# Kernel tuning notes

Measured on AMD Instinct MI355X. Metric: run time of the kernel, lower is better.

The kernel has to match this reference:

```python
import jax, jax.numpy as jnp
import numpy as np

DIM = 256
NPOINT = 64      # fps sample count (hardcoded in forward)
NSAMPLE = 8      # ball-query neighbors
RADIUS = 4.0
LN_EPS = 1e-5


def _fps(coor, K):
    # coor: [B,N,3] -> idx [B,K] int32, pointnet2-style (start at index 0)
    B, N, _ = coor.shape
    def step(carry, _):
        dists, far = carry
        c = jnp.take_along_axis(coor, far[:, None, None], axis=1)  # [B,1,3]
        d = jnp.sum((coor - c) ** 2, axis=-1)                      # [B,N]
        dists = jnp.minimum(dists, d)
        nxt = jnp.argmax(dists, axis=-1).astype(jnp.int32)
        return (dists, nxt), far
    init = (jnp.full((B, N), 1e10, coor.dtype), jnp.zeros((B,), jnp.int32))
    _, idx = jax.lax.scan(step, init, None, length=K)
    return idx.T  # [B,K]


def _ball_query(coor, centers, radius, nsample):
    # coor [B,N,3], centers [B,S,3] -> idx [B,S,nsample] (first-nsample within radius,
    # padded with the first hit, CUDA ball_query semantics)
    d2 = jnp.sum((centers[:, :, None, :] - coor[:, None, :, :]) ** 2, axis=-1)  # [B,S,N]
    mask = d2 < radius * radius
    cum = jnp.cumsum(mask.astype(jnp.int32), axis=-1)
    idxs, founds = [], []
    for j in range(nsample):  # fixed tiny loop
        sel = (cum == j + 1) & mask
        idxs.append(jnp.argmax(sel, axis=-1))
        founds.append(jnp.any(sel, axis=-1))
    idx = jnp.stack(idxs, axis=-1)       # [B,S,ns]
    found = jnp.stack(founds, axis=-1)
    return jnp.where(found, idx, idx[..., :1])


def _layernorm(v, g, b):
    m = jnp.mean(v, axis=-1, keepdims=True)
    var = jnp.mean((v - m) ** 2, axis=-1, keepdims=True)
    return (v - m) * jax.lax.rsqrt(var + LN_EPS) * g + b


def setup_inputs() -> dict:
    key = jax.random.key(0)
    ks = jax.random.split(key, 4)
    B, N = 8, 32768
    x = jax.random.normal(ks[0], (B, N, DIM), jnp.float32)
    coor = jax.random.normal(ks[1], (B, N, 3), jnp.float32)
    s = 1.0 / np.sqrt(DIM)
    Wq = jax.random.normal(ks[2], (DIM, DIM), jnp.float32) * s
    Wk = jax.random.normal(ks[3], (DIM, DIM), jnp.float32) * s
    return {
        "x": x, "coor": coor, "Wq": Wq, "Wk": Wk,
        "ln_q_g": jnp.ones((DIM,), jnp.float32), "ln_q_b": jnp.zeros((DIM,), jnp.float32),
        "ln_k_g": jnp.ones((DIM,), jnp.float32), "ln_k_b": jnp.zeros((DIM,), jnp.float32),
    }


def reference(x, coor, Wq, Wk, ln_q_g, ln_q_b, ln_k_g, ln_k_b):
    B, N, C = x.shape
    S = NPOINT
    bidx = jnp.arange(B)[:, None, None]

    fps_idx = _fps(coor, S)                              # [B,S]
    sample_coor = jnp.take_along_axis(coor, fps_idx[..., None], axis=1)  # [B,S,3]
    sample_x = jnp.take_along_axis(x, fps_idx[..., None], axis=1)        # [B,S,C]

    nidx = _ball_query(coor, sample_coor, RADIUS, NSAMPLE)  # [B,S,ns]
    grouped_xyz = coor[bidx, nidx]                          # [B,S,ns,3]
    grouped_feat = x[bidx, nidx]                            # [B,S,ns,C]
    local_coor = grouped_xyz - sample_coor[:, :, None, :]   # relative xyz [B,S,ns,3]

    global_x = jnp.max(grouped_feat, axis=2)                # [B,S,C]
    diff_x = global_x - sample_x                            # [B,S,C]
    diff_coor = jnp.mean(local_coor, axis=2)                # [B,S,3]

    # faithful reproduction of torch's view(B, NK, heads, -1) on a [B,3,S] tensor
    v = jnp.transpose(diff_coor, (0, 2, 1)).reshape(B, S, 3)  # memory reinterpretation

    q = _layernorm(diff_x, ln_q_g, ln_q_b) @ Wq.T           # [B,S,C]
    k = _layernorm(sample_x, ln_k_g, ln_k_b) @ Wk.T         # [B,S,C]
    scale = 1.0 / np.sqrt(DIM)  # head_dim = out_dim // 1
    attn = jax.nn.softmax(jnp.einsum('bnc,bmc->bnm', q, k) * scale, axis=-1)
    coor_2 = jnp.einsum('bnm,bmd->bnd', attn, v)            # [B,S,3]

    return (sample_x + diff_x, sample_coor + coor_2)
```

## Files before the change

### kernel.cpp

```cpp
#include <hip/hip_runtime.h>

#define BATCH 8
#define NPTS  32768
#define DIM   256
#define NSAMP 64
#define NNBR  8
#define LN_EPS 1e-5f

#define K_LDS    12
#define K_REG    12
#define K_STREAM 8

__device__ float g_sample_coor[BATCH * NSAMP * 3];
__device__ float g_diff_coor[BATCH * NSAMP * 3];
__device__ float g_qbuf[BATCH * NSAMP * DIM];
__device__ float g_kbuf[BATCH * NSAMP * DIM];
__device__ int   g_fidx[BATCH * NSAMP];


__device__ __forceinline__ double dist2_64(float px, float py, float pz,
                                           float cx, float cy, float cz) {
    double dx = (double)px - (double)cx;
    double dy = (double)py - (double)cy;
    double dz = (double)pz - (double)cz;
    return (dx * dx + dy * dy) + dz * dz;
}

__global__ __launch_bounds__(1024, 4) void fps_kernel(
    const float* __restrict__ coor)
{
    const int b = blockIdx.x;
    const int t = threadIdx.x;
    const float* cb = coor + (size_t)b * NPTS * 3;

    __shared__ float s_coor[K_LDS][1024][3];
    __shared__ float s_rv[16];
    __shared__ int   s_ri[16];
    __shared__ float s_ctr[3];

#pragma unroll
    for (int k = 0; k < K_LDS; ++k) {
        const int p = (k << 10) + t;
        s_coor[k][t][0] = cb[p * 3 + 0];
        s_coor[k][t][1] = cb[p * 3 + 1];
        s_coor[k][t][2] = cb[p * 3 + 2];
    }
    float px[K_REG], py[K_REG], pz[K_REG];
#pragma unroll
    for (int k = 0; k < K_REG; ++k) {
        const int p = ((K_LDS + k) << 10) + t;
        px[k] = cb[p * 3 + 0];
        py[k] = cb[p * 3 + 1];
        pz[k] = cb[p * 3 + 2];
    }

    float dist[32];
#pragma unroll
    for (int k = 0; k < 32; ++k) dist[k] = 1e10f;

    float cx = cb[0], cy = cb[1], cz = cb[2];
    int cidx = 0;
    __syncthreads();

    for (int s = 0; s < NSAMP; ++s) {
        if (t == 0) {
            g_fidx[b * NSAMP + s] = cidx;
            g_sample_coor[(b * NSAMP + s) * 3 + 0] = cx;
            g_sample_coor[(b * NSAMP + s) * 3 + 1] = cy;
            g_sample_coor[(b * NSAMP + s) * 3 + 2] = cz;
        }
        if (s == NSAMP - 1) break;

        float best = -1.0f; int bidx = 0;

#pragma unroll
        for (int k = 0; k < K_LDS; ++k) {
            float dx = s_coor[k][t][0] - cx;
            float dy = s_coor[k][t][1] - cy;
            float dz = s_coor[k][t][2] - cz;
            float d2 = dx * dx + dy * dy + dz * dz;
            float nd = fminf(dist[k], d2);
            dist[k] = nd;
            if (nd > best) { best = nd; bidx = (k << 10) + t; }
        }
#pragma unroll
        for (int k = 0; k < K_REG; ++k) {
            float dx = px[k] - cx;
            float dy = py[k] - cy;
            float dz = pz[k] - cz;
            float d2 = dx * dx + dy * dy + dz * dz;
            float nd = fminf(dist[K_LDS + k], d2);
            dist[K_LDS + k] = nd;
            if (nd > best) { best = nd; bidx = ((K_LDS + k) << 10) + t; }
        }
#pragma unroll 2
        for (int k = 0; k < K_STREAM; ++k) {
            const int p = ((K_LDS + K_REG + k) << 10) + t;
            float sx = cb[p * 3 + 0];
            float sy = cb[p * 3 + 1];
            float sz = cb[p * 3 + 2];
            float dx = sx - cx, dy = sy - cy, dz = sz - cz;
            float d2 = dx * dx + dy * dy + dz * dz;
            float nd = fminf(dist[K_LDS + K_REG + k], d2);
            dist[K_LDS + K_REG + k] = nd;
            if (nd > best) { best = nd; bidx = p; }
        }

#pragma unroll
        for (int off = 32; off > 0; off >>= 1) {
            float ov = __shfl_xor(best, off);
            int   oi = __shfl_xor(bidx, off);
            if (ov > best || (ov == best && oi < bidx)) { best = ov; bidx = oi; }
        }
        if ((t & 63) == 0) { s_rv[t >> 6] = best; s_ri[t >> 6] = bidx; }
        __syncthreads();

        if (t < 64) {
            float bv = (t < 16) ? s_rv[t] : -2.0f;
            int   bi = (t < 16) ? s_ri[t] : 0x7fffffff;
#pragma unroll
            for (int off = 8; off > 0; off >>= 1) {
                float ov = __shfl_xor(bv, off);
                int   oi = __shfl_xor(bi, off);
                if (ov > bv || (ov == bv && oi < bi)) { bv = ov; bi = oi; }
            }
            if (t == 0) {
                cidx = bi;
                s_ctr[0] = cb[bi * 3 + 0];
                s_ctr[1] = cb[bi * 3 + 1];
                s_ctr[2] = cb[bi * 3 + 2];
            }
        }
        __syncthreads();
        cx = s_ctr[0]; cy = s_ctr[1]; cz = s_ctr[2];
    }
}

__global__ __launch_bounds__(64) void ballquery_kernel(
    const float* __restrict__ coor,
    const float* __restrict__ x,
    float* __restrict__ out0)
{
    const int bid = blockIdx.x;
    const int b = bid >> 6, s = bid & 63;
    const int lane = threadIdx.x;
    const float* cb = coor + (size_t)b * NPTS * 3;

    const float cx = g_sample_coor[(b * NSAMP + s) * 3 + 0];
    const float cy = g_sample_coor[(b * NSAMP + s) * 3 + 1];
    const float cz = g_sample_coor[(b * NSAMP + s) * 3 + 2];

    __shared__ int s_nidx[NNBR];
    int found = 0;
    for (int ch = 0; ch < NPTS / 64 && found < NNBR; ++ch) {
        int p = (ch << 6) + lane;
        double d2 = dist2_64(cb[p * 3 + 0], cb[p * 3 + 1], cb[p * 3 + 2],
                             cx, cy, cz);
        unsigned long long m = __ballot(d2 < 16.0);
        while (m && found < NNBR) {
            int bpos = __ffsll(m) - 1;
            if (lane == 0) s_nidx[found] = (ch << 6) + bpos;
            ++found;
            m &= m - 1;
        }
    }
    if (lane == 0) {
        if (found == 0) { s_nidx[0] = 0; found = 1; }
        int f0 = s_nidx[0];
        for (int j = found; j < NNBR; ++j) s_nidx[j] = f0;
    }
    __syncthreads();

    int c0 = lane * 4;
    float a0 = -1e30f, a1 = -1e30f, a2 = -1e30f, a3 = -1e30f;
#pragma unroll
    for (int j = 0; j < NNBR; ++j) {
        const float4 v = *(const float4*)(x + ((size_t)b * NPTS + s_nidx[j]) * DIM + c0);
        a0 = fmaxf(a0, v.x); a1 = fmaxf(a1, v.y);
        a2 = fmaxf(a2, v.z); a3 = fmaxf(a3, v.w);
    }
    float4 o; o.x = a0; o.y = a1; o.z = a2; o.w = a3;
    *(float4*)(out0 + ((size_t)(b * NSAMP + s)) * DIM + c0) = o;

    if (lane < 3) {
        float sum = 0.f;
#pragma unroll
        for (int j = 0; j < NNBR; ++j) {
            float pv = cb[s_nidx[j] * 3 + lane];
            sum += pv - ((lane == 0) ? cx : (lane == 1) ? cy : cz);
        }
        g_diff_coor[(b * NSAMP + s) * 3 + lane] = sum * 0.125f;
    }
}

__global__ __launch_bounds__(256) void ln_gemm_kernel(
    const float* __restrict__ x,
    const float* __restrict__ out0,
    const float* __restrict__ Wq,
    const float* __restrict__ Wk,
    const float* __restrict__ gq, const float* __restrict__ bq,
    const float* __restrict__ gk, const float* __restrict__ bk)
{
    const int bid = blockIdx.x;
    const int which = bid & 1;
    const int s = (bid >> 1) & 63;
    const int b = bid >> 7;
    const int c = threadIdx.x;

    const int fidx = g_fidx[b * NSAMP + s];
    float xs = x[((size_t)b * NPTS + fidx) * DIM + c];
    float r  = which ? xs : (out0[(size_t)(b * NSAMP + s) * DIM + c] - xs);

    __shared__ float red[4];
    __shared__ float ln[DIM];

    float sum = r;
#pragma unroll
    for (int off = 32; off; off >>= 1) sum += __shfl_xor(sum, off);
    int wid = c >> 6;
    if ((c & 63) == 0) red[wid] = sum;
    __syncthreads();
    float mean = (red[0] + red[1] + red[2] + red[3]) * (1.0f / DIM);
    float d = r - mean;
    float vs = d * d;
#pragma unroll
    for (int off = 32; off; off >>= 1) vs += __shfl_xor(vs, off);
    __syncthreads();
    if ((c & 63) == 0) red[wid] = vs;
    __syncthreads();
    float var = (red[0] + red[1] + red[2] + red[3]) * (1.0f / DIM);
    float rs = 1.0f / sqrtf(var + LN_EPS);

    ln[c] = d * rs * (which ? gk[c] : gq[c]) + (which ? bk[c] : bq[c]);
    __syncthreads();

    const float* W = (which ? Wk : Wq) + (size_t)c * DIM;
    float acc = 0.f;
#pragma unroll 4
    for (int i = 0; i < DIM; i += 4) {
        float4 wv = *(const float4*)(W + i);
        acc = fmaf(ln[i + 0], wv.x, acc);
        acc = fmaf(ln[i + 1], wv.y, acc);
        acc = fmaf(ln[i + 2], wv.z, acc);
        acc = fmaf(ln[i + 3], wv.w, acc);
    }
    (which ? g_kbuf : g_qbuf)[(size_t)(b * NSAMP + s) * DIM + c] = acc;
}

__global__ __launch_bounds__(1024) void attn_kernel(
    float* __restrict__ out1)
{
    const int b = blockIdx.x;
    const int tid = threadIdx.x;
    __shared__ float att[64][64];
    __shared__ float vv[64][3];

    {
        const int i  = tid >> 4;
        const int j0 = (tid & 15) << 2;
        const float* qr = g_qbuf + (size_t)(b * NSAMP + i) * DIM;
        const float* k0 = g_kbuf + (size_t)(b * NSAMP + j0) * DIM;
        float a0 = 0, a1 = 0, a2 = 0, a3 = 0;
        for (int ii = 0; ii < DIM; ii += 4) {
            float4 qv = *(const float4*)(qr + ii);
            float4 v0 = *(const float4*)(k0 + ii);
            float4 v1 = *(const float4*)(k0 + DIM + ii);
            float4 v2 = *(const float4*)(k0 + 2 * DIM + ii);
            float4 v3 = *(const float4*)(k0 + 3 * DIM + ii);
            a0 += qv.x * v0.x + qv.y * v0.y + qv.z * v0.z + qv.w * v0.w;
            a1 += qv.x * v1.x + qv.y * v1.y + qv.z * v1.z + qv.w * v1.w;
            a2 += qv.x * v2.x + qv.y * v2.y + qv.z * v2.z + qv.w * v2.w;
            a3 += qv.x * v3.x + qv.y * v3.y + qv.z * v3.z + qv.w * v3.w;
        }
        att[i][j0 + 0] = a0 * 0.0625f;
        att[i][j0 + 1] = a1 * 0.0625f;
        att[i][j0 + 2] = a2 * 0.0625f;
        att[i][j0 + 3] = a3 * 0.0625f;
    }
    __syncthreads();

    const int wv_ = tid >> 6, lane = tid & 63;
    for (int r = wv_; r < 64; r += 16) {
        float v = att[r][lane];
        float m = v;
#pragma unroll
        for (int off = 32; off; off >>= 1) m = fmaxf(m, __shfl_xor(m, off));
        float e = expf(v - m);
        float ss = e;
#pragma unroll
        for (int off = 32; off; off >>= 1) ss += __shfl_xor(ss, off);
        att[r][lane] = e / ss;
    }
    if (tid < 192) {
        int m = tid / 3, d = tid - 3 * m;
        vv[m][d] = g_diff_coor[(size_t)(b * NSAMP + (tid & 63)) * 3 + (tid >> 6)];
    }
    __syncthreads();

    for (int r = wv_; r < 64; r += 16) {
        float a = att[r][lane];
        float s0 = a * vv[lane][0];
        float s1 = a * vv[lane][1];
        float s2 = a * vv[lane][2];
#pragma unroll
        for (int off = 32; off; off >>= 1) {
            s0 += __shfl_xor(s0, off);
            s1 += __shfl_xor(s1, off);
            s2 += __shfl_xor(s2, off);
        }
        if (lane == 0) {
            int o = (b * NSAMP + r) * 3;
            out1[o + 0] = g_sample_coor[o + 0] + s0;
            out1[o + 1] = g_sample_coor[o + 1] + s1;
            out1[o + 2] = g_sample_coor[o + 2] + s2;
        }
    }
}

extern "C" void kernel_launch(void* const* d_in, const int* in_sizes, int n_in,
                              void* d_out, int out_size, void* d_ws, size_t ws_size,
                              hipStream_t stream)
{
    const float* x    = (const float*)d_in[0];
    const float* coor = (const float*)d_in[1];
    if (in_sizes[0] == BATCH * NPTS * 3) {
        x    = (const float*)d_in[1];
        coor = (const float*)d_in[0];
    }
    const float* Wq   = (const float*)d_in[2];
    const float* Wk   = (const float*)d_in[3];
    const float* gq   = (const float*)d_in[4];
    const float* bq   = (const float*)d_in[5];
    const float* gk   = (const float*)d_in[6];
    const float* bk   = (const float*)d_in[7];

    float* out0 = (float*)d_out;
    float* out1 = out0 + (size_t)BATCH * NSAMP * DIM;

    hipLaunchKernelGGL(fps_kernel, dim3(BATCH), dim3(1024), 0, stream, coor);
    hipLaunchKernelGGL(ballquery_kernel, dim3(BATCH * NSAMP), dim3(64), 0, stream,
                       coor, x, out0);
    hipLaunchKernelGGL(ln_gemm_kernel, dim3(BATCH * NSAMP * 2), dim3(256), 0, stream,
                       x, out0, Wq, Wk, gq, bq, gk, bk);
    hipLaunchKernelGGL(attn_kernel, dim3(BATCH), dim3(1024), 0, stream, out1);
}
```

Before: 748.6 us.

## Stream FPS tail points with float4 loads instead of register caching

The farthest point sampling kernel no longer keeps 12 points per thread cached in registers. It now streams 20 points per thread from global memory on every iteration, using three float4 loads that cover four contiguous points per thread. A waves-per-EU attribute is added to pin occupancy. This frees registers and vectorises the loads, but each sampling iteration now reads more global or L2 data on a latency-bound serial loop.

Measured after the change: 1.116 ms. 49.0% more time.

```diff
diff --git a/kernel.cpp b/kernel.cpp
--- a/kernel.cpp
+++ b/kernel.cpp
@@ -8,8 +8,7 @@
 #define LN_EPS 1e-5f
 
 #define K_LDS    12
-#define K_REG    12
-#define K_STREAM 8
+#define K_STREAM 20
 
 __device__ float g_sample_coor[BATCH * NSAMP * 3];
 __device__ float g_diff_coor[BATCH * NSAMP * 3];
@@ -26,8 +25,9 @@
     return (dx * dx + dy * dy) + dz * dz;
 }
 
-__global__ __launch_bounds__(1024, 4) void fps_kernel(
-    const float* __restrict__ coor)
+__global__ __launch_bounds__(1024, 4)
+__attribute__((amdgpu_waves_per_eu(4, 4)))
+void fps_kernel(const float* __restrict__ coor)
 {
     const int b = blockIdx.x;
     const int t = threadIdx.x;
@@ -45,18 +45,12 @@
         s_coor[k][t][1] = cb[p * 3 + 1];
         s_coor[k][t][2] = cb[p * 3 + 2];
     }
-    float px[K_REG], py[K_REG], pz[K_REG];
-#pragma unroll
-    for (int k = 0; k < K_REG; ++k) {
-        const int p = ((K_LDS + k) << 10) + t;
-        px[k] = cb[p * 3 + 0];
-        py[k] = cb[p * 3 + 1];
-        pz[k] = cb[p * 3 + 2];
-    }
 
     float dist[32];
 #pragma unroll
     for (int k = 0; k < 32; ++k) dist[k] = 1e10f;
+
+    const float4* cb4 = (const float4*)(cb + 3 * (K_LDS << 10));
 
     float cx = cb[0], cy = cb[1], cz = cb[2];
     int cidx = 0;
@@ -83,27 +77,25 @@
             dist[k] = nd;
             if (nd > best) { best = nd; bidx = (k << 10) + t; }
         }
-#pragma unroll
-        for (int k = 0; k < K_REG; ++k) {
-            float dx = px[k] - cx;
-            float dy = py[k] - cy;
-            float dz = pz[k] - cz;
-            float d2 = dx * dx + dy * dy + dz * dz;
-            float nd = fminf(dist[K_LDS + k], d2);
-            dist[K_LDS + k] = nd;
-            if (nd > best) { best = nd; bidx = ((K_LDS + k) << 10) + t; }
-        }
 #pragma unroll 2
-        for (int k = 0; k < K_STREAM; ++k) {
-            const int p = ((K_LDS + K_REG + k) << 10) + t;
-            float sx = cb[p * 3 + 0];
-            float sy = cb[p * 3 + 1];
-            float sz = cb[p * 3 + 2];
-            float dx = sx - cx, dy = sy - cy, dz = sz - cz;
-            float d2 = dx * dx + dy * dy + dz * dz;
-            float nd = fminf(dist[K_LDS + K_REG + k], d2);
-            dist[K_LDS + K_REG + k] = nd;
-            if (nd > best) { best = nd; bidx = p; }
+        for (int j = 0; j < 5; ++j) {
+            const int g = (j << 10) + t;
+            const float4 v0 = cb4[g * 3 + 0];
+            const float4 v1 = cb4[g * 3 + 1];
+            const float4 v2 = cb4[g * 3 + 2];
+            const float qx[4] = { v0.x, v0.w, v1.z, v2.y };
+            const float qy[4] = { v0.y, v1.x, v1.w, v2.z };
+            const float qz[4] = { v0.z, v1.y, v2.x, v2.w };
+            const int pbase = (K_LDS << 10) + (g << 2);
+#pragma unroll
+            for (int i = 0; i < 4; ++i) {
+                float dx = qx[i] - cx, dy = qy[i] - cy, dz = qz[i] - cz;
+                float d2 = dx * dx + dy * dy + dz * dz;
+                const int di = K_LDS + (j << 2) + i;
+                float nd = fminf(dist[di], d2);
+                dist[di] = nd;
+                if (nd > best) { best = nd; bidx = pbase + i; }
+            }
         }
 
 #pragma unroll
```

## Split ball query into parallel mask pass and gather, streamline FPS reduction

Applied to the files above, without the earlier changes.

Ball query is split into two kernels. The first computes per-sample radius bitmasks across all point chunks in parallel (4096 blocks). The second scans those masks to find the first neighbours and gathers the features. This removes the serial per-sample chunk scan with its dependent global loads. FPS drops the register-cached points, moves one more slice into LDS and streams the rest from global. It also replaces the second barrier with a redundant all-thread final reduction that uses double-buffered shared slots, and reads the chosen centre from LDS. The cost is a 2 MB mask buffer plus an extra launch, and more global streaming per FPS iteration.

Result: slower. 870.0 us (+16.2%).

```diff
diff --git a/kernel.cpp b/kernel.cpp
--- a/kernel.cpp
+++ b/kernel.cpp
@@ -7,15 +7,15 @@
 #define NNBR  8
 #define LN_EPS 1e-5f
 
-#define K_LDS    12
-#define K_REG    12
-#define K_STREAM 8
+#define K_LDS    13
+#define K_STREAM 19
 
 __device__ float g_sample_coor[BATCH * NSAMP * 3];
 __device__ float g_diff_coor[BATCH * NSAMP * 3];
 __device__ float g_qbuf[BATCH * NSAMP * DIM];
 __device__ float g_kbuf[BATCH * NSAMP * DIM];
 __device__ int   g_fidx[BATCH * NSAMP];
+__device__ unsigned long long g_bmask[BATCH * NSAMP][NPTS / 64];
 
 
 __device__ __forceinline__ double dist2_64(float px, float py, float pz,
@@ -26,7 +26,7 @@
     return (dx * dx + dy * dy) + dz * dz;
 }
 
-__global__ __launch_bounds__(1024, 4) void fps_kernel(
+__global__ __launch_bounds__(1024) void fps_kernel(
     const float* __restrict__ coor)
 {
     const int b = blockIdx.x;
@@ -34,9 +34,8 @@
     const float* cb = coor + (size_t)b * NPTS * 3;
 
     __shared__ float s_coor[K_LDS][1024][3];
-    __shared__ float s_rv[16];
-    __shared__ int   s_ri[16];
-    __shared__ float s_ctr[3];
+    __shared__ float s_rv[2][16];
+    __shared__ int   s_ri[2][16];
 
 #pragma unroll
     for (int k = 0; k < K_LDS; ++k) {
@@ -44,14 +43,6 @@
         s_coor[k][t][0] = cb[p * 3 + 0];
         s_coor[k][t][1] = cb[p * 3 + 1];
         s_coor[k][t][2] = cb[p * 3 + 2];
-    }
-    float px[K_REG], py[K_REG], pz[K_REG];
-#pragma unroll
-    for (int k = 0; k < K_REG; ++k) {
-        const int p = ((K_LDS + k) << 10) + t;
-        px[k] = cb[p * 3 + 0];
-        py[k] = cb[p * 3 + 1];
-        pz[k] = cb[p * 3 + 2];
     }
 
     float dist[32];
@@ -83,26 +74,16 @@
             dist[k] = nd;
             if (nd > best) { best = nd; bidx = (k << 10) + t; }
         }
-#pragma unroll
-        for (int k = 0; k < K_REG; ++k) {
-            float dx = px[k] - cx;
-            float dy = py[k] - cy;
-            float dz = pz[k] - cz;
-            float d2 = dx * dx + dy * dy + dz * dz;
-            float nd = fminf(dist[K_LDS + k], d2);
-            dist[K_LDS + k] = nd;
-            if (nd > best) { best = nd; bidx = ((K_LDS + k) << 10) + t; }
-        }
-#pragma unroll 2
+#pragma unroll 4
         for (int k = 0; k < K_STREAM; ++k) {
-            const int p = ((K_LDS + K_REG + k) << 10) + t;
+            const int p = ((K_LDS + k) << 10) + t;
             float sx = cb[p * 3 + 0];
             float sy = cb[p * 3 + 1];
             float sz = cb[p * 3 + 2];
             float dx = sx - cx, dy = sy - cy, dz = sz - cz;
             float d2 = dx * dx + dy * dy + dz * dz;
-            float nd = fminf(dist[K_LDS + K_REG + k], d2);
-            dist[K_LDS + K_REG + k] = nd;
+            float nd = fminf(dist[K_LDS + k], d2);
+            dist[K_LDS + k] = nd;
             if (nd > best) { best = nd; bidx = p; }
         }
 
@@ -112,31 +93,56 @@
             int   oi = __shfl_xor(bidx, off);
             if (ov > best || (ov == best && oi < bidx)) { best = ov; bidx = oi; }
         }
-        if ((t & 63) == 0) { s_rv[t >> 6] = best; s_ri[t >> 6] = bidx; }
+        const int par = s & 1;
+        if ((t & 63) == 0) { s_rv[par][t >> 6] = best; s_ri[par][t >> 6] = bidx; }
         __syncthreads();
-
-        if (t < 64) {
-            float bv = (t < 16) ? s_rv[t] : -2.0f;
-            int   bi = (t < 16) ? s_ri[t] : 0x7fffffff;
-#pragma unroll
-            for (int off = 8; off > 0; off >>= 1) {
-                float ov = __shfl_xor(bv, off);
-                int   oi = __shfl_xor(bi, off);
-                if (ov > bv || (ov == bv && oi < bi)) { bv = ov; bi = oi; }
-            }
-            if (t == 0) {
-                cidx = bi;
-                s_ctr[0] = cb[bi * 3 + 0];
-                s_ctr[1] = cb[bi * 3 + 1];
-                s_ctr[2] = cb[bi * 3 + 2];
-            }
-        }
-        __syncthreads();
-        cx = s_ctr[0]; cy = s_ctr[1]; cz = s_ctr[2];
-    }
-}
-
-__global__ __launch_bounds__(64) void ballquery_kernel(
+        float bv = s_rv[par][t & 15];
+        int   bi = s_ri[par][t & 15];
+#pragma unroll
+        for (int off = 8; off > 0; off >>= 1) {
+            float ov = __shfl_xor(bv, off);
+            int   oi = __shfl_xor(bi, off);
+            if (ov > bv || (ov == bv && oi < bi)) { bv = ov; bi = oi; }
+        }
+        cidx = bi;
+        const int sl = bi >> 10, ix = bi & 1023;
+        if (sl < K_LDS) {
+            cx = s_coor[sl][ix][0];
+            cy = s_coor[sl][ix][1];
+            cz = s_coor[sl][ix][2];
+        } else {
+            cx = cb[bi * 3 + 0];
+            cy = cb[bi * 3 + 1];
+            cz = cb[bi * 3 + 2];
+        }
+    }
+}
+
+__global__ __launch_bounds__(64) void ballmask_kernel(
+    const float* __restrict__ coor)
+{
+    const int bid = blockIdx.x;
+    const int b   = bid >> 9;
+    const int ch  = bid & 511;
+    const int lane = threadIdx.x;
+    const float* cb = coor + (size_t)b * NPTS * 3;
+
+    const int p = (ch << 6) + lane;
+    const float px = cb[p * 3 + 0];
+    const float py = cb[p * 3 + 1];
+    const float pz = cb[p * 3 + 2];
+
+    const float* sc = g_sample_coor + b * NSAMP * 3;
+#pragma unroll 4
+    for (int s = 0; s < NSAMP; ++s) {
+        double d2 = dist2_64(px, py, pz, sc[s * 3 + 0], sc[s * 3 + 1],
+                             sc[s * 3 + 2]);
+        unsigned long long m = __ballot(d2 < 16.0);
+        if (lane == 0) g_bmask[b * NSAMP + s][ch] = m;
+    }
+}
+
+__global__ __launch_bounds__(64) void ballgather_kernel(
     const float* __restrict__ coor,
     const float* __restrict__ x,
     float* __restrict__ out0)
@@ -151,17 +157,23 @@
     const float cz = g_sample_coor[(b * NSAMP + s) * 3 + 2];
 
     __shared__ int s_nidx[NNBR];
+    const unsigned long long* mrow = g_bmask[b * NSAMP + s];
+
     int found = 0;
-    for (int ch = 0; ch < NPTS / 64 && found < NNBR; ++ch) {
-        int p = (ch << 6) + lane;
-        double d2 = dist2_64(cb[p * 3 + 0], cb[p * 3 + 1], cb[p * 3 + 2],
-                             cx, cy, cz);
-        unsigned long long m = __ballot(d2 < 16.0);
-        while (m && found < NNBR) {
-            int bpos = __ffsll(m) - 1;
-            if (lane == 0) s_nidx[found] = (ch << 6) + bpos;
-            ++found;
-            m &= m - 1;
+    for (int g = 0; g < (NPTS / 64) / 64 && found < NNBR; ++g) {
+        unsigned long long mym = mrow[(g << 6) + lane];
+        unsigned long long nz = __ballot(mym != 0ull);
+        while (nz && found < NNBR) {
+            int src = __ffsll(nz) - 1;
+            unsigned long long mv = __shfl(mym, src);
+            int pbase = (((g << 6) + src) << 6);
+            while (mv && found < NNBR) {
+                int bpos = __ffsll(mv) - 1;
+                if (lane == 0) s_nidx[found] = pbase + bpos;
+                ++found;
+                mv &= mv - 1;
+            }
+            nz &= nz - 1;
         }
     }
     if (lane == 0) {
@@ -338,7 +350,9 @@
     float* out1 = out0 + (size_t)BATCH * NSAMP * DIM;
 
     hipLaunchKernelGGL(fps_kernel, dim3(BATCH), dim3(1024), 0, stream, coor);
-    hipLaunchKernelGGL(ballquery_kernel, dim3(BATCH * NSAMP), dim3(64), 0, stream,
+    hipLaunchKernelGGL(ballmask_kernel, dim3(BATCH * (NPTS / 64)), dim3(64), 0,
+                       stream, coor);
+    hipLaunchKernelGGL(ballgather_kernel, dim3(BATCH * NSAMP), dim3(64), 0, stream,
                        coor, x, out0);
     hipLaunchKernelGGL(ln_gemm_kernel, dim3(BATCH * NSAMP * 2), dim3(256), 0, stream,
                        x, out0, Wq, Wk, gq, bq, gk, bk);
```
